# Performance work log

Hardware: AMD Instinct MI355X
Metric: run time of the kernel (lower is better)

## Reference

```python
import jax, jax.numpy as jnp
import numpy as np

DIM = 512
KEY_DIM = 32
NUM_HEADS = 8
ATTN_RATIO = 4
RES = 1024
B = 16
NH_KD = KEY_DIM * NUM_HEADS          # 256
D = ATTN_RATIO * KEY_DIM             # 128
DH = D * NUM_HEADS                   # 1024
H_QKV = DH + 2 * NH_KD               # 1536
EPS = 1e-5
SCALE = KEY_DIM ** -0.5


def bn(y, g, b, m, v):
    # eval-mode BatchNorm1d over channel dim of [B, C, L]
    inv = g / jnp.sqrt(v + EPS)
    return (y - m[None, :, None]) * inv[None, :, None] + b[None, :, None]


def setup_inputs() -> dict:
    key = jax.random.key(0)
    ks = jax.random.split(key, 16)
    x = jax.random.normal(ks[0], (B, DIM, RES), dtype=jnp.float32)
    w_qkv = jax.random.normal(ks[1], (H_QKV, DIM), dtype=jnp.float32) * 0.02
    qkv_g = jnp.ones((H_QKV,), jnp.float32)
    qkv_b = jnp.zeros((H_QKV,), jnp.float32)
    qkv_m = jax.random.normal(ks[2], (H_QKV,), jnp.float32) * 0.1
    qkv_v = jax.random.uniform(ks[3], (H_QKV,), jnp.float32) + 0.5
    w_dw = jax.random.normal(ks[4], (NH_KD, 1, 3), jnp.float32) * 0.1
    dw_g = jnp.ones((NH_KD,), jnp.float32)
    dw_b = jnp.zeros((NH_KD,), jnp.float32)
    dw_m = jax.random.normal(ks[5], (NH_KD,), jnp.float32) * 0.1
    dw_v = jax.random.uniform(ks[6], (NH_KD,), jnp.float32) + 0.5
    w_proj = jax.random.normal(ks[7], (DIM, DH), jnp.float32) * 0.02
    proj_g = jnp.ones((DIM,), jnp.float32)  # bn_weight_init=0 in source, use 1 for nontrivial output
    proj_b = jnp.zeros((DIM,), jnp.float32)
    proj_m = jax.random.normal(ks[8], (DIM,), jnp.float32) * 0.1
    proj_v = jax.random.uniform(ks[9], (DIM,), jnp.float32) + 0.5
    attention_biases = jax.random.normal(ks[10], (NUM_HEADS, RES), jnp.float32) * 0.02
    pts = jnp.arange(RES)
    bias_idxs = jnp.abs(pts[:, None] - pts[None, :]).astype(jnp.int32)  # [N, N]
    return dict(x=x, w_qkv=w_qkv, qkv_g=qkv_g, qkv_b=qkv_b, qkv_m=qkv_m, qkv_v=qkv_v,
                w_dw=w_dw, dw_g=dw_g, dw_b=dw_b, dw_m=dw_m, dw_v=dw_v,
                w_proj=w_proj, proj_g=proj_g, proj_b=proj_b, proj_m=proj_m, proj_v=proj_v,
                attention_biases=attention_biases, bias_idxs=bias_idxs)


def reference(x, w_qkv, qkv_g, qkv_b, qkv_m, qkv_v,
              w_dw, dw_g, dw_b, dw_m, dw_v,
              w_proj, proj_g, proj_b, proj_m, proj_v,
              attention_biases, bias_idxs):
    Bsz, _, L = x.shape
    # qkv: conv1x1 + BN
    qkv = bn(jnp.einsum('bcl,oc->bol', x, w_qkv), qkv_g, qkv_b, qkv_m, qkv_v)
    q = qkv[:, :NH_KD]
    k = qkv[:, NH_KD:2 * NH_KD]
    v = qkv[:, 2 * NH_KD:]
    # depthwise conv k=3 pad=1 on q, then BN
    q = jax.lax.conv_general_dilated(q, w_dw, window_strides=(1,), padding=((1, 1),),
                                     dimension_numbers=('NCH', 'OIH', 'NCH'),
                                     feature_group_count=NH_KD)
    q = bn(q, dw_g, dw_b, dw_m, dw_v)
    q = q.reshape(Bsz, NUM_HEADS, KEY_DIM, L)
    k = k.reshape(Bsz, NUM_HEADS, KEY_DIM, L)
    v = v.reshape(Bsz, NUM_HEADS, D, L)
    ab = attention_biases[:, bias_idxs]  # [H, N, N]
    attn = jnp.einsum('bhdn,bhdm->bhnm', q, k) * SCALE + ab[None]
    attn = jax.nn.softmax(attn, axis=-1)
    out = jnp.einsum('bhdm,bhnm->bhdn', v, attn).reshape(Bsz, DH, L)
    # proj: ReLU -> conv1x1 -> BN
    out = jax.nn.relu(out)
    out = bn(jnp.einsum('bcl,oc->bol', out, w_proj), proj_g, proj_b, proj_m, proj_v)
    return out
```

## Files before the change

### kernel.cpp

```cpp
#include <hip/hip_runtime.h>
#include <stdint.h>

#define DEV __device__ __forceinline__

typedef unsigned short u16;
typedef __bf16 bf16x8 __attribute__((ext_vector_type(8)));
typedef float floatx4 __attribute__((ext_vector_type(4)));
typedef unsigned short u16x4 __attribute__((ext_vector_type(4)));
typedef unsigned short u16x8 __attribute__((ext_vector_type(8)));
typedef short s16x4 __attribute__((ext_vector_type(4)));


DEV u16 f2bf(float x) {
  union { float f; uint32_t u; } v; v.f = x;
  uint32_t r = v.u + 0x7FFFu + ((v.u >> 16) & 1u);
  return (u16)(r >> 16);
}
DEV float bf2f(u16 x) {
  union { uint32_t u; float f; } v; v.u = ((uint32_t)x) << 16;
  return v.f;
}
DEV float loadf(const void* p, int i, int bf) {
  return bf ? bf2f(((const u16*)p)[i]) : ((const float*)p)[i];
}
DEV u16 fastbf(float x) {
  union { float f; uint32_t u; } v; v.f = x;
  return (u16)((v.u + 0x8000u) >> 16);
}

DEV floatx4 mfma16(bf16x8 a, bf16x8 b, floatx4 c) {
  return __builtin_amdgcn_mfma_f32_16x16x32_bf16(a, b, c, 0, 0, 0);
}

#if __has_builtin(__builtin_amdgcn_mfma_f32_16x16x16bf16_1k)
DEV floatx4 mfma16k16(s16x4 a, s16x4 b, floatx4 c) {
  return __builtin_amdgcn_mfma_f32_16x16x16bf16_1k(a, b, c, 0, 0, 0);
}
#elif __has_builtin(__builtin_amdgcn_mfma_f32_16x16x16_bf16)
DEV floatx4 mfma16k16(s16x4 a, s16x4 b, floatx4 c) {
  return __builtin_amdgcn_mfma_f32_16x16x16_bf16(a, b, c, 0, 0, 0);
}
#else
DEV floatx4 mfma16k16(s16x4 a, s16x4 b, floatx4 c) {
  asm volatile("v_mfma_f32_16x16x16_bf16 %0, %1, %2, %0"
               : "+v"(c) : "v"(a), "v"(b));
  return c;
}
#endif

DEV void gl_lds16(const void* g, void* l) {
  __builtin_amdgcn_global_load_lds(
      (const __attribute__((address_space(1))) void*)g,
      (__attribute__((address_space(3))) void*)l, 16, 0, 0);
}

__global__ void sniff(const uint32_t* __restrict__ x, int* __restrict__ flag) {
  int lane = threadIdx.x & 63;
  int hits = 0;
#pragma unroll
  for (int i = 0; i < 4; ++i) {
    uint32_t u = x[lane * 4 + i];
    int e = (u >> 7) & 0xFF;
    hits += (e >= 100 && e <= 140) ? 1 : 0;
  }
  unsigned long long m = __ballot(hits >= 3);
  if (lane == 0) *flag = (__popcll(m) >= 40) ? 1 : 0;
}

__global__ __launch_bounds__(256) void cvt_all(
    const void* __restrict__ a, const void* __restrict__ b,
    const void* __restrict__ c, const void* __restrict__ d,
    u16* __restrict__ oa, u16* __restrict__ ob, u16* __restrict__ oc,
    u16* __restrict__ od, const int* __restrict__ flag) {
  int i = blockIdx.x * 256 + threadIdx.x;
  int bf = *flag;
  if (i < 786432) {
    oa[i] = bf ? ((const u16*)a)[i] : f2bf(((const float*)a)[i]);
  } else if (i < 1310720) {
    int j = i - 786432;
    ob[j] = bf ? ((const u16*)b)[j] : f2bf(((const float*)b)[j]);
  } else if (i < 1311488) {
    int j = i - 1310720;
    oc[j] = bf ? ((const u16*)c)[j] : f2bf(((const float*)c)[j]);
  } else if (i < 1319680) {
    int j = i - 1311488;
    od[j] = bf ? ((const u16*)d)[j] : f2bf(((const float*)d)[j]);
  }
}

__global__ __launch_bounds__(256) void prep_params(
    const void* qg, const void* qb, const void* qm, const void* qv,
    const void* dg, const void* db, const void* dm, const void* dv,
    const void* pg, const void* pb, const void* pm, const void* pv,
    float* scl, float* shf, const int* __restrict__ flag) {
  int i = blockIdx.x * 256 + threadIdx.x;
  if (i >= 2304) return;
  int bf = *flag;
  float g, b, m, v;
  if (i < 1536)      { g = loadf(qg, i, bf); b = loadf(qb, i, bf); m = loadf(qm, i, bf); v = loadf(qv, i, bf); }
  else if (i < 1792) { int j = i - 1536; g = loadf(dg, j, bf); b = loadf(db, j, bf); m = loadf(dm, j, bf); v = loadf(dv, j, bf); }
  else               { int j = i - 1792; g = loadf(pg, j, bf); b = loadf(pb, j, bf); m = loadf(pm, j, bf); v = loadf(pv, j, bf); }
  float s = g / sqrtf(v + 1e-5f);
  scl[i] = s;
  shf[i] = b - m * s;
}

__global__ __launch_bounds__(256) void transpose_x(const void* __restrict__ x,
                                                   u16* __restrict__ xT,
                                                   const int* __restrict__ flag) {
  __shared__ __align__(16) u16 tile[64 * 72];
  const int tid = threadIdx.x;
  const int b = blockIdx.z, c0 = blockIdx.y * 64, l0 = blockIdx.x * 64;
  const int bf = *flag;
  const size_t base = ((size_t)b * 512 + c0) * 1024 + l0;
  if (bf) {
    const u16* xb = (const u16*)x + base;
#pragma unroll
    for (int it = 0; it < 4; ++it) {
      int flat = it * 256 + tid;
      int row = flat >> 4, c4 = flat & 15;
      u16x4 v = *(const u16x4*)(xb + (size_t)row * 1024 + c4 * 4);
      tile[(c4 * 4 + 0) * 72 + row] = v.x;
      tile[(c4 * 4 + 1) * 72 + row] = v.y;
      tile[(c4 * 4 + 2) * 72 + row] = v.z;
      tile[(c4 * 4 + 3) * 72 + row] = v.w;
    }
  } else {
    const float* xb = (const float*)x + base;
#pragma unroll
    for (int it = 0; it < 4; ++it) {
      int flat = it * 256 + tid;
      int row = flat >> 4, c4 = flat & 15;
      floatx4 v = *(const floatx4*)(xb + (size_t)row * 1024 + c4 * 4);
      tile[(c4 * 4 + 0) * 72 + row] = f2bf(v[0]);
      tile[(c4 * 4 + 1) * 72 + row] = f2bf(v[1]);
      tile[(c4 * 4 + 2) * 72 + row] = f2bf(v[2]);
      tile[(c4 * 4 + 3) * 72 + row] = f2bf(v[3]);
    }
  }
  __syncthreads();
  u16* xTb = xT + ((size_t)b * 1024 + l0) * 512 + c0;
#pragma unroll
  for (int it = 0; it < 4; ++it) {
    int flat = it * 256 + tid;
    int row = flat >> 4, c4 = flat & 15;
    u16x4 v = *(const u16x4*)&tile[row * 72 + c4 * 4];
    *(u16x4*)(xTb + (size_t)row * 512 + c4 * 4) = v;
  }
}

template <int K>
__global__ __launch_bounds__(256) void gemm_bn(
    const u16* __restrict__ A, const u16* __restrict__ BT, u16* __restrict__ Y,
    const float* __restrict__ scl, const float* __restrict__ shf, int sclOff,
    const int* __restrict__ flag, int outFlagged) {
  __shared__ __align__(16) u16 lds[4 * 64 * 72];
  const int tid = threadIdx.x, lane = tid & 63, w = tid >> 6;
  const int l15 = lane & 15, quad = lane >> 4;
  const int o_blk = blockIdx.y * 128, l_blk = blockIdx.x * 128, b = blockIdx.z;
  const int o_off = (w >> 1) * 64, l_off = (w & 1) * 64;
  const u16* BTb = BT + (size_t)b * 1024 * K;

  floatx4 acc[4][4];
#pragma unroll
  for (int i = 0; i < 4; ++i)
#pragma unroll
    for (int j = 0; j < 4; ++j) acc[i][j] = (floatx4){0.f, 0.f, 0.f, 0.f};

  for (int k0 = 0; k0 < K; k0 += 32) {
    __syncthreads();
#pragma unroll
    for (int s = 0; s < 2; ++s) {
      const int chunk = (s * 4 + w) * 1024;
      const int byteoff = chunk + lane * 16;
      const int row = byteoff >> 6;
      const int col = (byteoff & 63) >> 1;
      gl_lds16(A + (size_t)(o_blk + row) * K + k0 + col, &lds[chunk >> 1]);
      gl_lds16(BTb + (size_t)(l_blk + row) * K + k0 + col, &lds[4096 + (chunk >> 1)]);
    }
    __syncthreads();
    bf16x8 af[4], bfr[4];
#pragma unroll
    for (int ir = 0; ir < 4; ++ir)
      af[ir] = *(const bf16x8*)&lds[(o_off + 16 * ir + l15) * 32 + quad * 8];
#pragma unroll
    for (int jc = 0; jc < 4; ++jc)
      bfr[jc] = *(const bf16x8*)&lds[4096 + (l_off + 16 * jc + l15) * 32 + quad * 8];
#pragma unroll
    for (int ir = 0; ir < 4; ++ir)
#pragma unroll
      for (int jc = 0; jc < 4; ++jc)
        acc[ir][jc] = mfma16(af[ir], bfr[jc], acc[ir][jc]);
  }
  __syncthreads();
  u16* eb = &lds[w * 4608];
#pragma unroll
  for (int ir = 0; ir < 4; ++ir) {
#pragma unroll
    for (int r = 0; r < 4; ++r) {
      int rloc = 16 * ir + quad * 4 + r;
      int o = o_blk + o_off + rloc;
      float s = scl[sclOff + o], hh = shf[sclOff + o];
#pragma unroll
      for (int jc = 0; jc < 4; ++jc)
        eb[rloc * 72 + 16 * jc + l15] = f2bf(acc[ir][jc][r] * s + hh);
    }
  }
  asm volatile("s_waitcnt lgkmcnt(0)" ::: "memory");
  const int M = gridDim.y * 128;
  const size_t ybase = ((size_t)b * M + o_blk + o_off) * 1024 + l_blk + l_off;
  const int outbf = outFlagged ? *flag : 1;
  if (outbf) {
#pragma unroll
    for (int it = 0; it < 8; ++it) {
      int flat = it * 64 + lane;
      int row = flat >> 3, g = flat & 7;
      u16x8 v = *(const u16x8*)&eb[row * 72 + g * 8];
      *(u16x8*)(Y + ybase + (size_t)row * 1024 + g * 8) = v;
    }
  } else {
    float* Yf = (float*)Y;
#pragma unroll
    for (int it = 0; it < 8; ++it) {
      int flat = it * 64 + lane;
      int row = flat >> 3, g = flat & 7;
      u16x8 v = *(const u16x8*)&eb[row * 72 + g * 8];
      floatx4 lo, hi;
#pragma unroll
      for (int t = 0; t < 4; ++t) { lo[t] = bf2f(v[t]); hi[t] = bf2f(v[4 + t]); }
      *(floatx4*)(Yf + ybase + (size_t)row * 1024 + g * 8) = lo;
      *(floatx4*)(Yf + ybase + (size_t)row * 1024 + g * 8 + 4) = hi;
    }
  }
}

__global__ __launch_bounds__(256) void dwconv_pack(
    const u16* __restrict__ qkv, const u16* __restrict__ w_dw,
    const float* __restrict__ scl, const float* __restrict__ shf,
    u16* __restrict__ qT, u16* __restrict__ kT) {
  __shared__ __align__(16) u16 lds[256 * 36];
  const int tid = threadIdx.x;
  const int lch = blockIdx.x, h = blockIdx.y, b = blockIdx.z;
  const int r = tid >> 3, seg = tid & 7;
  const int l0 = lch * 256 + seg * 32;
  {
    const int o = h * 32 + r;
    const u16* base = qkv + ((size_t)b * 1536 + o) * 1024;
    float w0 = bf2f(w_dw[o * 3 + 0]), w1 = bf2f(w_dw[o * 3 + 1]), w2 = bf2f(w_dw[o * 3 + 2]);
    float sc = scl[1536 + o], sh = shf[1536 + o];
    float prev = (l0 > 0) ? bf2f(base[l0 - 1]) : 0.f;
    float cur = bf2f(base[l0]);
#pragma unroll 4
    for (int j = 0; j < 32; ++j) {
      int lg = l0 + j;
      float nxt = (lg + 1 < 1024) ? bf2f(base[lg + 1]) : 0.f;
      lds[(seg * 32 + j) * 36 + r] = f2bf((w0 * prev + w1 * cur + w2 * nxt) * sc + sh);
      prev = cur; cur = nxt;
    }
  }
  __syncthreads();
  {
    const size_t qTb = (((size_t)b * 8 + h) * 1024 + lch * 256) * 32;
#pragma unroll
    for (int it = 0; it < 8; ++it) {
      int flat = it * 256 + tid;
      int ll = flat >> 3, g = flat & 7;
      u16x4 v = *(const u16x4*)&lds[ll * 36 + g * 4];
      *(u16x4*)(qT + qTb + (size_t)ll * 32 + g * 4) = v;
    }
  }
  __syncthreads();
  {
    const int o = 256 + h * 32 + r;
    const u16* base = qkv + ((size_t)b * 1536 + o) * 1024;
#pragma unroll 8
    for (int j = 0; j < 32; ++j) lds[(seg * 32 + j) * 36 + r] = base[l0 + j];
  }
  __syncthreads();
  {
    const size_t kTb = (((size_t)b * 8 + h) * 1024 + lch * 256) * 32;
#pragma unroll
    for (int it = 0; it < 8; ++it) {
      int flat = it * 256 + tid;
      int ll = flat >> 3, g = flat & 7;
      u16x4 v = *(const u16x4*)&lds[ll * 36 + g * 4];
      *(u16x4*)(kT + kTb + (size_t)ll * 32 + g * 4) = v;
    }
  }
}

__global__ __launch_bounds__(512, 4) void attn(
    const u16* __restrict__ qT, const u16* __restrict__ kT,
    const u16* __restrict__ qkv, const u16* __restrict__ ab,
    u16* __restrict__ OT) {
  __shared__ __align__(16) float biasE[2048];
  __shared__ __align__(16) u16 ldsV[2 * 4096];
  const int tid = threadIdx.x, lane = tid & 63, w = tid >> 6;
  const int l15 = lane & 15, quad = lane >> 4;
  const int id = blockIdx.x;
  const int pair = id & 127, nb = id >> 7;
  const int b = pair >> 3, h = pair & 7;
  for (int i = tid; i < 2048; i += 512) {
    int dd = i - 1024;
    int idx = dd < 0 ? -dd : dd;
    if (idx > 1023) idx = 1023;
    biasE[i] = bf2f(ab[h * 1024 + idx]) * 1.44269504088896340f;
  }
  const int n0 = nb * 128 + w * 16;
  const size_t bh = ((size_t)b * 8 + h) * 1024;
  const u16* kTb = kT + bh * 32;
  const u16* vb = qkv + ((size_t)b * 1536 + 512 + h * 128) * 1024;
  const bf16x8 qf = *(const bf16x8*)(qT + bh * 32 + (size_t)(n0 + l15) * 32 + quad * 8);
  const int d = tid >> 2, sc = tid & 3;
  const u16* sg = vb + (size_t)d * 1024 + sc * 8;
  const int wb = (((d >> 4) * 4 + 2 * (sc & 1)) * 16 + (d & 15)) * 8 + (sc >> 1) * 4;

  floatx4 oacc[8];
#pragma unroll
  for (int j = 0; j < 8; ++j) oacc[j] = (floatx4){0.f, 0.f, 0.f, 0.f};
  float rs = 0.f;
  constexpr float c1 = 0.17677669529663689f * 1.44269504088896340f;
  const floatx4 zf = (floatx4){0.f, 0.f, 0.f, 0.f};

  const u16* kfp = kTb + (size_t)l15 * 32 + quad * 8;

  {
    u16x8 a = *(const u16x8*)sg;
    *(u16x4*)&ldsV[wb]       = (u16x4){a[0], a[1], a[2], a[3]};
    *(u16x4*)&ldsV[wb + 128] = (u16x4){a[4], a[5], a[6], a[7]};
  }
  __syncthreads();

#pragma unroll 1
  for (int m0 = 0; m0 < 1024; m0 += 32) {
    const int par = (m0 >> 5) & 1;
    const bool more = (m0 + 32) < 1024;
    u16x8 a;
    if (more) {
      a = *(const u16x8*)(sg + m0 + 32);
    }
    bf16x8 kf0 = *(const bf16x8*)(kfp + (size_t)m0 * 32);
    bf16x8 kf1 = *(const bf16x8*)(kfp + (size_t)(m0 + 16) * 32);
    floatx4 s0 = mfma16(kf0, qf, zf);
    floatx4 s1 = mfma16(kf1, qf, zf);
    const int Cb = 1024 + n0 + l15 - quad * 4 - m0;
    s16x4 pf0, pf1;
#pragma unroll
    for (int r = 0; r < 4; ++r) {
      float p0 = __builtin_amdgcn_exp2f(s0[r] * c1 + biasE[Cb - r]);
      float p1 = __builtin_amdgcn_exp2f(s1[r] * c1 + biasE[Cb - 16 - r]);
      rs += p0 + p1;
      pf0[r] = (short)fastbf(p0);
      pf1[r] = (short)fastbf(p1);
    }
    const int rbase = par * 4096 + quad * 128 + l15 * 8;
#pragma unroll
    for (int jd = 0; jd < 8; ++jd) {
      u16x8 vv = *(const u16x8*)&ldsV[rbase + jd * 512];
      s16x4 v0 = {(short)vv[0], (short)vv[1], (short)vv[2], (short)vv[3]};
      s16x4 v1 = {(short)vv[4], (short)vv[5], (short)vv[6], (short)vv[7]};
      oacc[jd] = mfma16k16(v0, pf0, oacc[jd]);
      oacc[jd] = mfma16k16(v1, pf1, oacc[jd]);
    }
    if (more) {
      u16* dst = ldsV + (par ^ 1) * 4096;
      *(u16x4*)&dst[wb]       = (u16x4){a[0], a[1], a[2], a[3]};
      *(u16x4*)&dst[wb + 128] = (u16x4){a[4], a[5], a[6], a[7]};
    }
    __syncthreads();
  }
  rs += __shfl_xor(rs, 16, 64);
  rs += __shfl_xor(rs, 32, 64);
  const float inv = __builtin_amdgcn_rcpf(rs);
  u16* OTb = OT + ((size_t)b * 1024 + n0 + l15) * 1024 + h * 128 + quad * 4;
#pragma unroll
  for (int jd = 0; jd < 8; ++jd) {
    u16x4 o;
#pragma unroll
    for (int r = 0; r < 4; ++r) {
      float v = oacc[jd][r] * inv;
      o[r] = fastbf(v > 0.f ? v : 0.f);
    }
    *(u16x4*)(OTb + 16 * jd) = o;
  }
}

extern "C" void kernel_launch(void* const* d_in, const int* in_sizes, int n_in,
                              void* d_out, int out_size, void* d_ws, size_t ws_size,
                              hipStream_t stream) {
  const void* x      = d_in[0];
  const void* w_qkv  = d_in[1];
  const void* qkv_g  = d_in[2];
  const void* qkv_b  = d_in[3];
  const void* qkv_m  = d_in[4];
  const void* qkv_v  = d_in[5];
  const void* w_dw   = d_in[6];
  const void* dw_g   = d_in[7];
  const void* dw_b   = d_in[8];
  const void* dw_m   = d_in[9];
  const void* dw_v   = d_in[10];
  const void* w_proj = d_in[11];
  const void* proj_g = d_in[12];
  const void* proj_b = d_in[13];
  const void* proj_m = d_in[14];
  const void* proj_v = d_in[15];
  const void* abias  = d_in[16];

  char* ws = (char*)d_ws;
  u16*   xT      = (u16*)(ws);
  u16*   qkv     = (u16*)(ws + 16777216);
  u16*   qT      = (u16*)(ws + 67108864);
  u16*   kT      = (u16*)(ws + 75497472);
  u16*   OT      = (u16*)(ws + 83886080);
  float* scl     = (float*)(ws + 117440512);
  float* shf     = (float*)(ws + 117449728);
  u16*   wqkv_c  = (u16*)(ws + 117458944);
  u16*   wproj_c = (u16*)(ws + 119031808);
  u16*   wdw_c   = (u16*)(ws + 120080384);
  u16*   ab_c    = (u16*)(ws + 120082432);
  int*   flag    = (int*)(ws + 120098816);
  if (ws_size < (size_t)120098880) return;

  sniff<<<1, 64, 0, stream>>>((const uint32_t*)x, flag);
  cvt_all<<<5155, 256, 0, stream>>>(w_qkv, w_proj, w_dw, abias,
                                    wqkv_c, wproj_c, wdw_c, ab_c, flag);
  prep_params<<<9, 256, 0, stream>>>(qkv_g, qkv_b, qkv_m, qkv_v, dw_g, dw_b, dw_m,
                                     dw_v, proj_g, proj_b, proj_m, proj_v, scl, shf, flag);
  transpose_x<<<dim3(16, 8, 16), 256, 0, stream>>>(x, xT, flag);
  gemm_bn<512><<<dim3(8, 12, 16), 256, 0, stream>>>(wqkv_c, xT, qkv, scl, shf, 0, flag, 0);
  dwconv_pack<<<dim3(4, 8, 16), 256, 0, stream>>>(qkv, wdw_c, scl, shf, qT, kT);
  attn<<<1024, 512, 0, stream>>>(qT, kT, qkv, ab_c, OT);
  gemm_bn<1024><<<dim3(8, 4, 16), 256, 0, stream>>>(wproj_c, OT, (u16*)d_out, scl, shf, 1792, flag, 1);
}
```

Before: 274.0 us.

## Use K=32 MFMA for PV with permuted key rows and padded V tile

Replaces the pair of 16x16x16 bf16 MFMAs per V tile with a single 16x16x32 MFMA. The key rows feeding the QK^T score MFMAs are permuted so each lane's eight probabilities already line up with the K=32 operand layout. The V tile in LDS now uses a padded row-major layout (stride 40), so each thread does one 16-byte store and one 16-byte read per tile instead of split 8-byte accesses. K fragments for the next step are prefetched into registers one iteration ahead. The aim is to halve the PV MFMA instruction count and cut LDS traffic, at the cost of more LDS and more live registers.

Measured after the change: 271.3 us. About the same (-1.0%).

```diff
diff --git a/kernel.cpp b/kernel.cpp
--- a/kernel.cpp
+++ b/kernel.cpp
@@ -27,26 +27,13 @@
   union { float f; uint32_t u; } v; v.f = x;
   return (u16)((v.u + 0x8000u) >> 16);
 }
+DEV bf16x8 u2b(u16x8 v) {
+  union { u16x8 u; bf16x8 b; } x; x.u = v; return x.b;
+}
 
 DEV floatx4 mfma16(bf16x8 a, bf16x8 b, floatx4 c) {
   return __builtin_amdgcn_mfma_f32_16x16x32_bf16(a, b, c, 0, 0, 0);
 }
-
-#if __has_builtin(__builtin_amdgcn_mfma_f32_16x16x16bf16_1k)
-DEV floatx4 mfma16k16(s16x4 a, s16x4 b, floatx4 c) {
-  return __builtin_amdgcn_mfma_f32_16x16x16bf16_1k(a, b, c, 0, 0, 0);
-}
-#elif __has_builtin(__builtin_amdgcn_mfma_f32_16x16x16_bf16)
-DEV floatx4 mfma16k16(s16x4 a, s16x4 b, floatx4 c) {
-  return __builtin_amdgcn_mfma_f32_16x16x16_bf16(a, b, c, 0, 0, 0);
-}
-#else
-DEV floatx4 mfma16k16(s16x4 a, s16x4 b, floatx4 c) {
-  asm volatile("v_mfma_f32_16x16x16_bf16 %0, %1, %2, %0"
-               : "+v"(c) : "v"(a), "v"(b));
-  return c;
-}
-#endif
 
 DEV void gl_lds16(const void* g, void* l) {
   __builtin_amdgcn_global_load_lds(
@@ -294,7 +281,7 @@
     const u16* __restrict__ qkv, const u16* __restrict__ ab,
     u16* __restrict__ OT) {
   __shared__ __align__(16) float biasE[2048];
-  __shared__ __align__(16) u16 ldsV[2 * 4096];
+  __shared__ __align__(16) u16 ldsV[2 * 5120];
   const int tid = threadIdx.x, lane = tid & 63, w = tid >> 6;
   const int l15 = lane & 15, quad = lane >> 4;
   const int id = blockIdx.x;
@@ -311,9 +298,13 @@
   const u16* kTb = kT + bh * 32;
   const u16* vb = qkv + ((size_t)b * 1536 + 512 + h * 128) * 1024;
   const bf16x8 qf = *(const bf16x8*)(qT + bh * 32 + (size_t)(n0 + l15) * 32 + quad * 8);
-  const int d = tid >> 2, sc = tid & 3;
-  const u16* sg = vb + (size_t)d * 1024 + sc * 8;
-  const int wb = (((d >> 4) * 4 + 2 * (sc & 1)) * 16 + (d & 15)) * 8 + (sc >> 1) * 4;
+  const int prow = 8 * (l15 >> 2) + (l15 & 3);
+  const u16* kfp0 = kTb + (size_t)prow * 32 + quad * 8;
+  const u16* kfp1 = kfp0 + 4 * 32;
+  const int sd = tid >> 2, sc = tid & 3;
+  const u16* sg = vb + (size_t)sd * 1024 + sc * 8;
+  const int wv = sd * 40 + sc * 8;
+  const int vrd = l15 * 40 + quad * 8;
 
   floatx4 oacc[8];
 #pragma unroll
@@ -322,12 +313,11 @@
   constexpr float c1 = 0.17677669529663689f * 1.44269504088896340f;
   const floatx4 zf = (floatx4){0.f, 0.f, 0.f, 0.f};
 
-  const u16* kfp = kTb + (size_t)l15 * 32 + quad * 8;
-
+  bf16x8 kc0 = *(const bf16x8*)(kfp0);
+  bf16x8 kc1 = *(const bf16x8*)(kfp1);
   {
     u16x8 a = *(const u16x8*)sg;
-    *(u16x4*)&ldsV[wb]       = (u16x4){a[0], a[1], a[2], a[3]};
-    *(u16x4*)&ldsV[wb + 128] = (u16x4){a[4], a[5], a[6], a[7]};
+    *(u16x8*)&ldsV[wv] = a;
   }
   __syncthreads();
 
@@ -336,36 +326,35 @@
     const int par = (m0 >> 5) & 1;
     const bool more = (m0 + 32) < 1024;
     u16x8 a;
+    bf16x8 kn0, kn1;
     if (more) {
       a = *(const u16x8*)(sg + m0 + 32);
-    }
-    bf16x8 kf0 = *(const bf16x8*)(kfp + (size_t)m0 * 32);
-    bf16x8 kf1 = *(const bf16x8*)(kfp + (size_t)(m0 + 16) * 32);
-    floatx4 s0 = mfma16(kf0, qf, zf);
-    floatx4 s1 = mfma16(kf1, qf, zf);
-    const int Cb = 1024 + n0 + l15 - quad * 4 - m0;
-    s16x4 pf0, pf1;
+      kn0 = *(const bf16x8*)(kfp0 + (size_t)(m0 + 32) * 32);
+      kn1 = *(const bf16x8*)(kfp1 + (size_t)(m0 + 32) * 32);
+    }
+    floatx4 s0 = mfma16(kc0, qf, zf);
+    floatx4 s1 = mfma16(kc1, qf, zf);
+    const int Cb = 1024 + n0 + l15 - 8 * quad - m0;
+    u16x8 pf;
 #pragma unroll
     for (int r = 0; r < 4; ++r) {
       float p0 = __builtin_amdgcn_exp2f(s0[r] * c1 + biasE[Cb - r]);
-      float p1 = __builtin_amdgcn_exp2f(s1[r] * c1 + biasE[Cb - 16 - r]);
+      float p1 = __builtin_amdgcn_exp2f(s1[r] * c1 + biasE[Cb - 4 - r]);
       rs += p0 + p1;
-      pf0[r] = (short)fastbf(p0);
-      pf1[r] = (short)fastbf(p1);
-    }
-    const int rbase = par * 4096 + quad * 128 + l15 * 8;
+      pf[r] = fastbf(p0);
+      pf[4 + r] = fastbf(p1);
+    }
+    const bf16x8 pfb = u2b(pf);
+    const int rbase = par * 5120 + vrd;
 #pragma unroll
     for (int jd = 0; jd < 8; ++jd) {
-      u16x8 vv = *(const u16x8*)&ldsV[rbase + jd * 512];
-      s16x4 v0 = {(short)vv[0], (short)vv[1], (short)vv[2], (short)vv[3]};
-      s16x4 v1 = {(short)vv[4], (short)vv[5], (short)vv[6], (short)vv[7]};
-      oacc[jd] = mfma16k16(v0, pf0, oacc[jd]);
-      oacc[jd] = mfma16k16(v1, pf1, oacc[jd]);
+      bf16x8 vv = *(const bf16x8*)&ldsV[rbase + jd * 640];
+      oacc[jd] = mfma16(vv, pfb, oacc[jd]);
     }
     if (more) {
-      u16* dst = ldsV + (par ^ 1) * 4096;
-      *(u16x4*)&dst[wb]       = (u16x4){a[0], a[1], a[2], a[3]};
-      *(u16x4*)&dst[wb + 128] = (u16x4){a[4], a[5], a[6], a[7]};
+      *(u16x8*)&ldsV[(par ^ 1) * 5120 + wv] = a;
+      kc0 = kn0;
+      kc1 = kn1;
     }
     __syncthreads();
   }
```
